# Optimization experiments

Hardware: AMD Instinct MI355X
Metric: run time of the kernel (lower is better)

## Reference

```python
import jax, jax.numpy as jnp
import numpy as np

L, B, D, H = 2048, 2, 1024, 16
HD = D // H
DFF = 4 * D
EPS = 1e-5


def layernorm(x, g, b):
    mu = jnp.mean(x, axis=-1, keepdims=True)
    var = jnp.mean((x - mu) ** 2, axis=-1, keepdims=True)
    return (x - mu) * jax.lax.rsqrt(var + EPS) * g + b


def setup_inputs() -> dict:
    key = jax.random.key(0)
    ks = jax.random.split(key, 12)
    s = 0.02
    return {
        "x": jax.random.normal(ks[0], (L, B, D), jnp.float32),
        "ln1_g": jnp.ones((D,), jnp.float32),
        "ln1_b": jnp.zeros((D,), jnp.float32),
        "w_attn": jax.random.normal(ks[1], (D, 3 * D), jnp.float32) * s,
        "b_attn": jnp.zeros((3 * D,), jnp.float32),
        "w_proj": jax.random.normal(ks[2], (D, D), jnp.float32) * s,
        "b_proj": jnp.zeros((D,), jnp.float32),
        "ln2_g": jnp.ones((D,), jnp.float32),
        "ln2_b": jnp.zeros((D,), jnp.float32),
        "w_fc": jax.random.normal(ks[3], (D, DFF), jnp.float32) * s,
        "b_fc": jnp.zeros((DFF,), jnp.float32),
        "w_out": jax.random.normal(ks[4], (DFF, D), jnp.float32) * s,
        "b_out": jnp.zeros((D,), jnp.float32),
    }


def reference(x, ln1_g, ln1_b, w_attn, b_attn, w_proj, b_proj,
              ln2_g, ln2_b, w_fc, b_fc, w_out, b_out):
    # x: [L, B, D]
    h = layernorm(x, ln1_g, ln1_b)
    qkv = h @ w_attn + b_attn                     # [L, B, 3D]
    qkv = jnp.transpose(qkv, (1, 0, 2))            # [B, L, 3D]
    q, k, v = jnp.split(qkv, 3, axis=-1)

    def split_heads(t):                            # [B, L, D] -> [B, H, L, hd]
        return jnp.transpose(t.reshape(B, L, H, HD), (0, 2, 1, 3))

    q, k, v = split_heads(q), split_heads(k), split_heads(v)
    # present: stack of (key, value), key in [B,H,L,hd] layout (post transpose-back)
    present = jnp.stack((k, v))                    # [2, B, H, L, hd]

    scores = jnp.einsum('bhqd,bhkd->bhqk', q, k) / jnp.sqrt(jnp.float32(HD))
    w = jax.nn.softmax(scores, axis=-1)
    a = jnp.einsum('bhqk,bhkd->bhqd', w, v)        # [B, H, L, hd]
    a = jnp.transpose(a, (0, 2, 1, 3)).reshape(B, L, D)
    a = a @ w_proj + b_proj                        # [B, L, D]
    a = jnp.transpose(a, (1, 0, 2))                # [L, B, D]

    x = x + a
    m = jax.nn.gelu(layernorm(x, ln2_g, ln2_b) @ w_fc + b_fc) @ w_out + b_out
    x = x + m
    return x, present
```

## Files before the change

kernel.cpp:

```cpp
#include <hip/hip_runtime.h>
#include <stdint.h>

#define L_SEQ 2048
#define BATCH 2
#define DIM   1024
#define NH    16
#define HDIM  64
#define DFF_  4096
#define ROWS  (L_SEQ*BATCH)

#define QSCALE 0.18033688011112042f

typedef __attribute__((ext_vector_type(8))) short  bf16x8;
typedef __attribute__((ext_vector_type(4))) float  floatx4;

__device__ __forceinline__ unsigned short f2bf(float f) {
    union { float f; uint32_t u; } x; x.f = f;
    uint32_t r = x.u + 0x7fffu + ((x.u >> 16) & 1u);
    return (unsigned short)(r >> 16);
}
__device__ __forceinline__ float bf2f(unsigned short b) {
    union { uint32_t u; float f; } x; x.u = ((uint32_t)b) << 16;
    return x.f;
}
__device__ __forceinline__ uint32_t fbits(float f) {
    union { float f; uint32_t u; } x; x.f = f; return x.u;
}

__device__ __forceinline__ void load_lds16(const unsigned short* g, unsigned short* l) {
    __builtin_amdgcn_global_load_lds(
        (const __attribute__((address_space(1))) unsigned int*)g,
        (__attribute__((address_space(3))) unsigned int*)l, 16, 0, 0);
}

__global__ __launch_bounds__(256)
void transpose_all(const float* __restrict__ s0, unsigned short* __restrict__ d0,
                   const float* __restrict__ s1, unsigned short* __restrict__ d1,
                   const float* __restrict__ s2, unsigned short* __restrict__ d2,
                   const float* __restrict__ s3, unsigned short* __restrict__ d3)
{
    const int id = blockIdx.x;
    const float* src; unsigned short* dst; int K, N, local;
    if (id < 3072)      { src = s0; dst = d0; K = 1024; N = 3072; local = id; }
    else if (id < 4096) { src = s1; dst = d1; K = 1024; N = 1024; local = id - 3072; }
    else if (id < 8192) { src = s2; dst = d2; K = 1024; N = 4096; local = id - 4096; }
    else                { src = s3; dst = d3; K = 4096; N = 1024; local = id - 8192; }
    const int nN = N >> 5;
    const int bk = (local / nN) * 32, bn = (local % nN) * 32;

    __shared__ float tile[32][36];
    const int t = threadIdx.x;
    const int r = t >> 3, c4 = (t & 7) * 4;
    *(float4*)&tile[r][c4] = *(const float4*)(src + (size_t)(bk + r) * N + bn + c4);
    __syncthreads();
    ushort4 o;
    o.x = f2bf(tile[c4 + 0][r]);
    o.y = f2bf(tile[c4 + 1][r]);
    o.z = f2bf(tile[c4 + 2][r]);
    o.w = f2bf(tile[c4 + 3][r]);
    *(ushort4*)(dst + (size_t)(bn + r) * K + bk + c4) = o;
}

template<int INBF16>
__global__ __launch_bounds__(256)
void ln_rows(const void* __restrict__ xin, const float* __restrict__ g,
             const float* __restrict__ bta, unsigned short* __restrict__ out)
{
    const int row = blockIdx.x;
    const int t = threadIdx.x;
    float4 v;
    if (INBF16) {
        const ushort4 u = ((const ushort4*)((const unsigned short*)xin + (size_t)row * DIM))[t];
        v.x = bf2f(u.x); v.y = bf2f(u.y); v.z = bf2f(u.z); v.w = bf2f(u.w);
    } else {
        v = ((const float4*)((const float*)xin + (size_t)row * DIM))[t];
    }
    float s  = v.x + v.y + v.z + v.w;
    float s2 = v.x*v.x + v.y*v.y + v.z*v.z + v.w*v.w;
#pragma unroll
    for (int d = 1; d < 64; d <<= 1) { s += __shfl_xor(s, d, 64); s2 += __shfl_xor(s2, d, 64); }
    __shared__ float ss[4], ss2[4];
    const int w = t >> 6, lane = t & 63;
    if (lane == 0) { ss[w] = s; ss2[w] = s2; }
    __syncthreads();
    s  = ss[0] + ss[1] + ss[2] + ss[3];
    s2 = ss2[0] + ss2[1] + ss2[2] + ss2[3];
    const float mu   = s * (1.0f / DIM);
    const float var  = s2 * (1.0f / DIM) - mu * mu;
    const float rstd = rsqrtf(var + 1e-5f);
    const float4 gv = ((const float4*)g)[t];
    const float4 bv = ((const float4*)bta)[t];
    ushort4 o;
    o.x = f2bf((v.x - mu) * rstd * gv.x + bv.x);
    o.y = f2bf((v.y - mu) * rstd * gv.y + bv.y);
    o.z = f2bf((v.z - mu) * rstd * gv.z + bv.z);
    o.w = f2bf((v.w - mu) * rstd * gv.w + bv.w);
    *(ushort4*)(out + (size_t)row * DIM + t * 4) = o;
}

template<int GELU, int RESID, int OUTBF16, int MI, int SPLITK>
__global__ __launch_bounds__(256)
void gemm_bt(const unsigned short* __restrict__ A,
             const unsigned short* __restrict__ Bt,
             const float* __restrict__ bias,
             const void* __restrict__ resid,
             void* __restrict__ outp,
             float* __restrict__ part,
             int M, int N, int K)
{
    __shared__ unsigned short As[MI * 32 * 32];
    __shared__ unsigned short Bs[128 * 32];
    const int t = threadIdx.x;
    const int w = t >> 6, lane = t & 63;
    const int quad = lane >> 4, l16 = lane & 15;
    const int wm = (w >> 1) * (MI * 16), wn = (w & 1) * 64;
    const int bm = blockIdx.x * (MI * 32), bn = blockIdx.y * 128;

    const int srow = lane >> 2;
    const int scol = (lane & 3) * 8;

    const unsigned short* Ab = A  + (size_t)bm * K;
    const unsigned short* Bb = Bt + (size_t)bn * K;

    floatx4 acc[MI][4] = {};

    const int kspan = (SPLITK > 1) ? (K / SPLITK) : K;
    const int k0    = (SPLITK > 1) ? blockIdx.z * kspan : 0;

    for (int kc = k0; kc < k0 + kspan; kc += 32) {
        __syncthreads();
#pragma unroll
        for (int i = 0; i < MI / 2; ++i) {
            const int r0 = (i * 4 + w) * 16;
            load_lds16(Ab + (size_t)(r0 + srow) * K + kc + scol, As + r0 * 32);
        }
#pragma unroll
        for (int i = 0; i < 2; ++i) {
            const int r0 = (i * 4 + w) * 16;
            load_lds16(Bb + (size_t)(r0 + srow) * K + kc + scol, Bs + r0 * 32);
        }
        __syncthreads();
        bf16x8 af[MI], bf[4];
#pragma unroll
        for (int i = 0; i < MI; ++i) af[i] = *(const bf16x8*)(As + (wm + i*16 + l16) * 32 + quad * 8);
#pragma unroll
        for (int j = 0; j < 4; ++j) bf[j] = *(const bf16x8*)(Bs + (wn + j*16 + l16) * 32 + quad * 8);
#pragma unroll
        for (int i = 0; i < MI; ++i)
#pragma unroll
            for (int j = 0; j < 4; ++j)
                acc[i][j] = __builtin_amdgcn_mfma_f32_16x16x32_bf16(af[i], bf[j], acc[i][j], 0, 0, 0);
    }

    if (SPLITK > 1 && blockIdx.z > 0) {
        float* po = part + (size_t)(blockIdx.z - 1) * ((size_t)M * N);
#pragma unroll
        for (int i = 0; i < MI; ++i)
#pragma unroll
            for (int j = 0; j < 4; ++j) {
                const int col = bn + wn + j*16 + l16;
#pragma unroll
                for (int r = 0; r < 4; ++r) {
                    const int row = bm + wm + i*16 + quad*4 + r;
                    po[(size_t)row * N + col] = acc[i][j][r];
                }
            }
        return;
    }

#pragma unroll
    for (int i = 0; i < MI; ++i) {
#pragma unroll
        for (int j = 0; j < 4; ++j) {
            const int col = bn + wn + j*16 + l16;
            const float bv = bias[col];
#pragma unroll
            for (int r = 0; r < 4; ++r) {
                const int row = bm + wm + i*16 + quad*4 + r;
                float v = acc[i][j][r] + bv;
                if (RESID == 1) v += ((const float*)resid)[(size_t)row * N + col];
                if (RESID == 2) v += bf2f(((const unsigned short*)resid)[(size_t)row * N + col]);
                if (GELU) {
                    const float u = v;
                    float c = 2.302204225929898f * (u + 0.044715f * u * u * u);
                    c = fminf(c, 80.f);
                    const float e = exp2f(c);
                    v = u * (e / (1.0f + e));
                }
                if (OUTBF16) ((unsigned short*)outp)[(size_t)row * N + col] = f2bf(v);
                else         ((float*)outp)[(size_t)row * N + col] = v;
            }
        }
    }
}

__global__ __launch_bounds__(256)
void splitk_add(const float* __restrict__ part, float* __restrict__ outp)
{
    const size_t i = ((size_t)blockIdx.x * 256 + threadIdx.x) * 4;
    float4 a = *(const float4*)(outp + i);
    const float4 p = *(const float4*)(part + i);
    a.x += p.x; a.y += p.y; a.z += p.z; a.w += p.w;
    *(float4*)(outp + i) = a;
}

__global__ __launch_bounds__(256)
void split_qkv(const unsigned short* __restrict__ qkv,
               unsigned short* __restrict__ q, unsigned short* __restrict__ k,
               float* __restrict__ present)
{
    const size_t idx = (size_t)blockIdx.x * 256 + threadIdx.x;
    const int g8  = idx & 7;
    const int l   = (idx >> 3) & 2047;
    const int bh  = (idx >> 14) & 31;
    const int sel = (int)(idx >> 19);
    const int b = bh >> 4, h = bh & 15;
    const unsigned short* src = qkv + (size_t)(l * BATCH + b) * (3 * DIM) + sel * DIM + h * HDIM + g8 * 8;
    const uint4 val = *(const uint4*)src;
    const unsigned short* sv = (const unsigned short*)&val;
    if (sel == 0) {
        unsigned short ov[8];
#pragma unroll
        for (int j = 0; j < 8; ++j) ov[j] = f2bf(bf2f(sv[j]) * QSCALE);
        *(uint4*)(q + ((size_t)bh * L_SEQ + l) * HDIM + g8 * 8) = *(uint4*)ov;
    } else {
        *(uint4*)(k + ((size_t)bh * L_SEQ + l) * HDIM + g8 * 8) = val;
        float* p = present + (((size_t)b * NH + h) * L_SEQ + l) * HDIM + (size_t)g8 * 8;
        float4 f0, f1;
        f0.x = bf2f(sv[0]); f0.y = bf2f(sv[1]); f0.z = bf2f(sv[2]); f0.w = bf2f(sv[3]);
        f1.x = bf2f(sv[4]); f1.y = bf2f(sv[5]); f1.z = bf2f(sv[6]); f1.w = bf2f(sv[7]);
        ((float4*)p)[0] = f0; ((float4*)p)[1] = f1;
    }
}

__global__ __launch_bounds__(256)
void transpose_v(const unsigned short* __restrict__ qkv, unsigned short* __restrict__ vt,
                 float* __restrict__ present)
{
    __shared__ unsigned short tile[64][72];
    const int lt = blockIdx.x;
    const int bh = blockIdx.y;
    const int b = bh >> 4, h = bh & 15;
    const int t = threadIdx.x;
#pragma unroll
    for (int i = 0; i < 2; ++i) {
        const int idx = i * 256 + t;
        const int l = idx >> 3, c = (idx & 7) * 8;
        const uint4 val =
            *(const uint4*)(qkv + (size_t)((lt * 64 + l) * BATCH + b) * (3 * DIM) + 2 * DIM + h * HDIM + c);
        *(uint4*)(&tile[l][c]) = val;
        const unsigned short* sv = (const unsigned short*)&val;
        float* p = present + ((((size_t)BATCH + b) * NH + h) * L_SEQ + lt * 64 + l) * HDIM + c;
        float4 f0, f1;
        f0.x = bf2f(sv[0]); f0.y = bf2f(sv[1]); f0.z = bf2f(sv[2]); f0.w = bf2f(sv[3]);
        f1.x = bf2f(sv[4]); f1.y = bf2f(sv[5]); f1.z = bf2f(sv[6]); f1.w = bf2f(sv[7]);
        ((float4*)p)[0] = f0; ((float4*)p)[1] = f1;
    }
    __syncthreads();
#pragma unroll
    for (int i = 0; i < 2; ++i) {
        const int idx = i * 256 + t;
        const int d = idx >> 3, l0 = (idx & 7) * 8;
        const int kk = l0 >> 3;
        ushort4 o[2];
        unsigned short* ov = (unsigned short*)o;
#pragma unroll
        for (int jj = 0; jj < 8; ++jj) {
            const int j = (jj + kk) & 7;
            ov[j] = tile[l0 + j][d];
        }
        *(uint4*)(vt + ((size_t)bh * HDIM + d) * L_SEQ + lt * 64 + l0) = *(uint4*)o;
    }
}

__global__ __launch_bounds__(256, 4)
void attn_kernel(const unsigned short* __restrict__ Q,
                 const unsigned short* __restrict__ Kk,
                 const unsigned short* __restrict__ Vt,
                 unsigned short* __restrict__ Opart,
                 float* __restrict__ Lpart)
{
    const int qt = blockIdx.x;
    const int ks = blockIdx.y;
    const int bh = blockIdx.z;
    const int b = bh >> 4, h = bh & 15;
    const int t = threadIdx.x, w = t >> 6, lane = t & 63;
    const int quad = lane >> 4, l16 = lane & 15;

    __shared__ unsigned short Ks[64][72];
    __shared__ unsigned short Vts[64][72];
    __shared__ unsigned short Ps[4][32][72];

    const size_t head_off = (size_t)bh * L_SEQ * HDIM;
    const int q_base = qt * 128 + w * 32;
    const int kt0 = ks * 1024;

    bf16x8 qf[2][2];
#pragma unroll
    for (int nf = 0; nf < 2; ++nf)
#pragma unroll
        for (int ds = 0; ds < 2; ++ds)
            qf[nf][ds] = *(const bf16x8*)(Q + head_off + (size_t)(q_base + nf*16 + l16) * HDIM + ds*32 + quad*8);

    const int sr = t >> 3;
    const int sc = (t & 7) * 8;

    floatx4 o[4][2] = {};
    float l_i[2] = {0.f, 0.f};

    for (int kt = kt0; kt < kt0 + 1024; kt += 64) {
        __syncthreads();
#pragma unroll
        for (int i = 0; i < 2; ++i) {
            const int row = sr + i * 32;
            *(uint4*)(&Ks[row][sc])  = *(const uint4*)(Kk + head_off + (size_t)(kt + row) * HDIM + sc);
            *(uint4*)(&Vts[row][sc]) = *(const uint4*)(Vt + head_off + (size_t)row * L_SEQ + kt + sc);
        }
        __syncthreads();

        floatx4 s[4][2] = {};
#pragma unroll
        for (int ds = 0; ds < 2; ++ds)
#pragma unroll
            for (int jt = 0; jt < 4; ++jt) {
                const bf16x8 kf = *(const bf16x8*)(&Ks[jt*16 + l16][ds*32 + quad*8]);
                s[jt][0] = __builtin_amdgcn_mfma_f32_16x16x32_bf16(kf, qf[0][ds], s[jt][0], 0, 0, 0);
                s[jt][1] = __builtin_amdgcn_mfma_f32_16x16x32_bf16(kf, qf[1][ds], s[jt][1], 0, 0, 0);
            }

#pragma unroll
        for (int nf = 0; nf < 2; ++nf)
#pragma unroll
            for (int jt = 0; jt < 4; ++jt) {
                const float p0 = exp2f(s[jt][nf][0]);
                const float p1 = exp2f(s[jt][nf][1]);
                const float p2 = exp2f(s[jt][nf][2]);
                const float p3 = exp2f(s[jt][nf][3]);
                l_i[nf] += (p0 + p1) + (p2 + p3);
                uint2 pk;
                pk.x = __builtin_amdgcn_perm(fbits(p1), fbits(p0), 0x07060302u);
                pk.y = __builtin_amdgcn_perm(fbits(p3), fbits(p2), 0x07060302u);
                *(uint2*)(&Ps[w][nf*16 + l16][jt*16 + quad*4]) = pk;
            }

#pragma unroll
        for (int kk = 0; kk < 2; ++kk) {
            const bf16x8 pf0 = *(const bf16x8*)(&Ps[w][l16]     [kk*32 + quad*8]);
            const bf16x8 pf1 = *(const bf16x8*)(&Ps[w][16 + l16][kk*32 + quad*8]);
#pragma unroll
            for (int dt = 0; dt < 4; ++dt) {
                const bf16x8 vf = *(const bf16x8*)(&Vts[dt*16 + l16][kk*32 + quad*8]);
                o[dt][0] = __builtin_amdgcn_mfma_f32_16x16x32_bf16(vf, pf0, o[dt][0], 0, 0, 0);
                o[dt][1] = __builtin_amdgcn_mfma_f32_16x16x32_bf16(vf, pf1, o[dt][1], 0, 0, 0);
            }
        }
    }

    unsigned short* Op = Opart + (size_t)ks * ROWS * DIM;
#pragma unroll
    for (int nf = 0; nf < 2; ++nf) {
        float l = l_i[nf];
        l += __shfl_xor(l, 16, 64);
        l += __shfl_xor(l, 32, 64);
        const int q = q_base + nf*16 + l16;
        if (quad == 0)
            Lpart[((size_t)ks * 32 + bh) * L_SEQ + q] = l;
#pragma unroll
        for (int dt = 0; dt < 4; ++dt) {
            ushort4 ov;
            ov.x = f2bf(o[dt][nf][0]); ov.y = f2bf(o[dt][nf][1]);
            ov.z = f2bf(o[dt][nf][2]); ov.w = f2bf(o[dt][nf][3]);
            *(ushort4*)(Op + (size_t)(q * BATCH + b) * DIM + h * HDIM + dt*16 + quad*4) = ov;
        }
    }
}

__global__ __launch_bounds__(256)
void attn_merge(const unsigned short* __restrict__ Opart,
                const float* __restrict__ Lpart,
                unsigned short* __restrict__ Aout)
{
    const int row = blockIdx.x;
    const int q = row >> 1, b = row & 1;
    const int t = threadIdx.x;
    const int col = t * 4;
    const int h = col >> 6;
    const int bh = b * 16 + h;
    const float l0 = Lpart[(size_t)bh * L_SEQ + q];
    const float l1 = Lpart[((size_t)32 + bh) * L_SEQ + q];
    const float inv = 1.0f / (l0 + l1);
    const ushort4 o0 = *(const ushort4*)(Opart + (size_t)row * DIM + col);
    const ushort4 o1 = *(const ushort4*)(Opart + (size_t)ROWS * DIM + (size_t)row * DIM + col);
    ushort4 ov;
    ov.x = f2bf((bf2f(o0.x) + bf2f(o1.x)) * inv);
    ov.y = f2bf((bf2f(o0.y) + bf2f(o1.y)) * inv);
    ov.z = f2bf((bf2f(o0.z) + bf2f(o1.z)) * inv);
    ov.w = f2bf((bf2f(o0.w) + bf2f(o1.w)) * inv);
    *(ushort4*)(Aout + (size_t)row * DIM + col) = ov;
}

extern "C" void kernel_launch(void* const* d_in, const int* in_sizes, int n_in,
                              void* d_out, int out_size, void* d_ws, size_t ws_size,
                              hipStream_t stream)
{
    const float* x      = (const float*)d_in[0];
    const float* ln1_g  = (const float*)d_in[1];
    const float* ln1_b  = (const float*)d_in[2];
    const float* w_attn = (const float*)d_in[3];
    const float* b_attn = (const float*)d_in[4];
    const float* w_proj = (const float*)d_in[5];
    const float* b_proj = (const float*)d_in[6];
    const float* ln2_g  = (const float*)d_in[7];
    const float* ln2_b  = (const float*)d_in[8];
    const float* w_fc   = (const float*)d_in[9];
    const float* b_fc   = (const float*)d_in[10];
    const float* w_out  = (const float*)d_in[11];
    const float* b_out  = (const float*)d_in[12];

    char* ws = (char*)d_ws;
    unsigned short* watT   = (unsigned short*)(ws + 0);
    unsigned short* wprojT = (unsigned short*)(ws + 6291456);
    unsigned short* wfcT   = (unsigned short*)(ws + 8388608);
    unsigned short* woutT  = (unsigned short*)(ws + 16777216);
    unsigned short* h      = (unsigned short*)(ws + 25165824);
    unsigned short* qkv    = (unsigned short*)(ws + 33554432);
    unsigned short* opart  = (unsigned short*)(ws + 33554432);
    float*          lpart  = (float*)(ws + 50331648);
    unsigned short* mws    = (unsigned short*)(ws + 33554432);
    unsigned short* qw     = (unsigned short*)(ws + 58720256);
    unsigned short* kw     = (unsigned short*)(ws + 67108864);
    unsigned short* vt     = (unsigned short*)(ws + 75497472);
    unsigned short* aw     = (unsigned short*)(ws + 83886080);
    unsigned short* x2     = (unsigned short*)(ws + 92274688);
    float*          kpart  = (float*)(ws + 75497472);

    float* xout    = (float*)d_out;
    float* present = (float*)d_out + 4194304;

    transpose_all<<<12288, 256, 0, stream>>>(w_attn, watT, w_proj, wprojT, w_fc, wfcT, w_out, woutT);

    ln_rows<0><<<ROWS, 256, 0, stream>>>(x, ln1_g, ln1_b, h);
    gemm_bt<0,0,1,4,1><<<dim3(32, 24), 256, 0, stream>>>(h, watT, b_attn, nullptr, qkv, nullptr, ROWS, 3*DIM, DIM);
    split_qkv<<<4096, 256, 0, stream>>>(qkv, qw, kw, present);
    transpose_v<<<dim3(32, 32), 256, 0, stream>>>(qkv, vt, present);
    attn_kernel<<<dim3(16, 2, 32), 256, 0, stream>>>(qw, kw, vt, opart, lpart);
    attn_merge<<<ROWS, 256, 0, stream>>>(opart, lpart, aw);
    gemm_bt<0,1,1,2,1><<<dim3(64, 8), 256, 0, stream>>>(aw, wprojT, b_proj, x, x2, nullptr, ROWS, DIM, DIM);
    ln_rows<1><<<ROWS, 256, 0, stream>>>(x2, ln2_g, ln2_b, h);
    gemm_bt<1,0,1,4,1><<<dim3(32, 32), 256, 0, stream>>>(h, wfcT, b_fc, nullptr, mws, nullptr, ROWS, DFF_, DIM);
    gemm_bt<0,2,0,4,2><<<dim3(32, 8, 2), 256, 0, stream>>>(mws, woutT, b_out, x2, xout, kpart, ROWS, DIM, DFF_);
    splitk_add<<<4096, 256, 0, stream>>>(kpart, xout);
}
```

Baseline: 418.6 us.

## Add 256x256-tile 8-wave pipelined GEMM for QKV and FC projections

Adds a new bf16 GEMM kernel with 256x256 output tiles, 512 threads, 128KB of double-buffered LDS with an XOR swizzle, and direct global-to-LDS loads. The K loop is split into four phases that interleave staging of the next tile with MFMA clusters, using priority raising and explicit waitcnt/barriers. Blocks are remapped so neighbouring workgroups are spread across XCDs. It replaces the QKV and FC GEMMs when the large dynamic LDS attribute can be set, aiming for higher data reuse and compute/load overlap, at the cost of one block per CU and only 192 or 256 blocks per launch.

Result: slower. 431.3 us (+3.0%).

```diff
diff --git a/kernel.cpp b/kernel.cpp
--- a/kernel.cpp
+++ b/kernel.cpp
@@ -194,6 +194,178 @@
     }
 }
 
+#define SWZ(p) ((p) ^ ((((p) >> 9) & 1) << 5))
+
+template<int GELU>
+__global__ __launch_bounds__(512)
+void gemm256(const unsigned short* __restrict__ A,
+             const unsigned short* __restrict__ Bt,
+             const float* __restrict__ bias,
+             unsigned short* __restrict__ outp,
+             int M, int N, int K, int nbx)
+{
+    extern __shared__ unsigned short lds[];
+    const int t = threadIdx.x;
+    const int w = t >> 6, lane = t & 63;
+    const int quad = lane >> 4, l16 = lane & 15;
+    const int wr = w >> 2, wc = w & 3;
+
+    const int nwg = gridDim.x;
+    const int cpx = nwg >> 3;
+    const int bid = (blockIdx.x & 7) * cpx + (blockIdx.x >> 3);
+    const int bm = (bid % nbx) * 256, bn = (bid / nbx) * 256;
+
+    const unsigned short* Ab = A  + (size_t)bm * K;
+    const unsigned short* Bb = Bt + (size_t)bn * K;
+
+    const int q0 = t * 16,        s0 = SWZ(q0);
+    const int q1 = (512 + t) * 16, s1 = SWZ(q1);
+    const int srow0 = s0 >> 7, scol0 = (s0 & 127) >> 1;
+    const int srow1 = s1 >> 7, scol1 = (s1 & 127) >> 1;
+
+#define STAGE(cb_, kt_, half_) do {                                                   \
+        const unsigned short* sb_ = ((half_) >= 2 ? Ab : Bb)                          \
+            + (size_t)(((half_) & 1) * 128) * K + (kt_) * 64;                         \
+        unsigned short* db_ = lds + (cb_) * 32768 + ((half_) >= 2 ? 0 : 16384)        \
+            + ((half_) & 1) * 8192 + w * 512;                                         \
+        load_lds16(sb_ + (size_t)srow0 * K + scol0, db_);                             \
+        load_lds16(sb_ + (size_t)srow1 * K + scol1, db_ + 4096);                      \
+    } while (0)
+
+#define PHASE_BAR  do { __builtin_amdgcn_s_barrier(); asm volatile("" ::: "memory"); } while (0)
+#define CL_PRE  do { asm volatile("s_waitcnt lgkmcnt(0)" ::: "memory"); \
+                     __builtin_amdgcn_sched_barrier(0); __builtin_amdgcn_s_setprio(1); } while (0)
+#define CL_POST do { __builtin_amdgcn_s_setprio(0); __builtin_amdgcn_sched_barrier(0); } while (0)
+
+    floatx4 acc[8][4] = {};
+    bf16x8 af[4][2], bf[4][2];
+    const int nt = K >> 6;
+
+    STAGE(0, 0, 0); STAGE(0, 0, 1); STAGE(0, 0, 2); STAGE(0, 0, 3);
+    STAGE(1, 1, 0);
+    asm volatile("s_waitcnt vmcnt(2)" ::: "memory");
+    PHASE_BAR;
+
+    for (int kt = 0; kt < nt; ++kt) {
+        const int cb = kt & 1;
+        const unsigned short* Al = lds + cb * 32768;
+        const unsigned short* Bl = lds + cb * 32768 + 16384;
+
+#pragma unroll
+        for (int mi = 0; mi < 4; ++mi)
+#pragma unroll
+            for (int ks = 0; ks < 2; ++ks) {
+                int p = (wr*128 + mi*16 + l16) * 128 + ks*64 + quad*16;
+                af[mi][ks] = *(const bf16x8*)((const char*)Al + SWZ(p));
+            }
+#pragma unroll
+        for (int nj = 0; nj < 4; ++nj)
+#pragma unroll
+            for (int ks = 0; ks < 2; ++ks) {
+                int p = (wc*64 + nj*16 + l16) * 128 + ks*64 + quad*16;
+                bf[nj][ks] = *(const bf16x8*)((const char*)Bl + SWZ(p));
+            }
+        if (kt + 1 < nt) STAGE((kt + 1) & 1, kt + 1, 1);
+        PHASE_BAR;
+        CL_PRE;
+#pragma unroll
+        for (int mi = 0; mi < 4; ++mi)
+#pragma unroll
+            for (int nj = 0; nj < 2; ++nj)
+#pragma unroll
+                for (int ks = 0; ks < 2; ++ks)
+                    acc[mi][nj] = __builtin_amdgcn_mfma_f32_16x16x32_bf16(af[mi][ks], bf[nj][ks], acc[mi][nj], 0, 0, 0);
+        CL_POST;
+        PHASE_BAR;
+
+        if (kt + 1 < nt) STAGE((kt + 1) & 1, kt + 1, 2);
+        PHASE_BAR;
+        CL_PRE;
+#pragma unroll
+        for (int mi = 0; mi < 4; ++mi)
+#pragma unroll
+            for (int nj = 2; nj < 4; ++nj)
+#pragma unroll
+                for (int ks = 0; ks < 2; ++ks)
+                    acc[mi][nj] = __builtin_amdgcn_mfma_f32_16x16x32_bf16(af[mi][ks], bf[nj][ks], acc[mi][nj], 0, 0, 0);
+        CL_POST;
+        PHASE_BAR;
+
+#pragma unroll
+        for (int mi = 0; mi < 4; ++mi)
+#pragma unroll
+            for (int ks = 0; ks < 2; ++ks) {
+                int p = (wr*128 + 64 + mi*16 + l16) * 128 + ks*64 + quad*16;
+                af[mi][ks] = *(const bf16x8*)((const char*)Al + SWZ(p));
+            }
+        if (kt + 1 < nt) STAGE((kt + 1) & 1, kt + 1, 3);
+        PHASE_BAR;
+        CL_PRE;
+#pragma unroll
+        for (int mi = 0; mi < 4; ++mi)
+#pragma unroll
+            for (int nj = 0; nj < 2; ++nj)
+#pragma unroll
+                for (int ks = 0; ks < 2; ++ks)
+                    acc[4 + mi][nj] = __builtin_amdgcn_mfma_f32_16x16x32_bf16(af[mi][ks], bf[nj][ks], acc[4 + mi][nj], 0, 0, 0);
+        CL_POST;
+        PHASE_BAR;
+
+        if (kt + 2 < nt) STAGE(cb, kt + 2, 0);
+        PHASE_BAR;
+        CL_PRE;
+#pragma unroll
+        for (int mi = 0; mi < 4; ++mi)
+#pragma unroll
+            for (int nj = 2; nj < 4; ++nj)
+#pragma unroll
+                for (int ks = 0; ks < 2; ++ks)
+                    acc[4 + mi][nj] = __builtin_amdgcn_mfma_f32_16x16x32_bf16(af[mi][ks], bf[nj][ks], acc[4 + mi][nj], 0, 0, 0);
+        CL_POST;
+        if (kt + 2 < nt)      { asm volatile("s_waitcnt vmcnt(2)" ::: "memory"); }
+        else if (kt + 1 < nt) { asm volatile("s_waitcnt vmcnt(0)" ::: "memory"); }
+        PHASE_BAR;
+    }
+
+#pragma unroll
+    for (int mi = 0; mi < 8; ++mi) {
+#pragma unroll
+        for (int nj = 0; nj < 4; ++nj) {
+            const int col = bn + wc*64 + nj*16 + l16;
+            const float bv = bias[col];
+#pragma unroll
+            for (int r = 0; r < 4; ++r) {
+                const int row = bm + wr*128 + mi*16 + quad*4 + r;
+                float v = acc[mi][nj][r] + bv;
+                if (GELU) {
+                    const float u = v;
+                    float c = 2.302204225929898f * (u + 0.044715f * u * u * u);
+                    c = fminf(c, 80.f);
+                    const float e = exp2f(c);
+                    v = u * (e / (1.0f + e));
+                }
+                outp[(size_t)row * N + col] = f2bf(v);
+            }
+        }
+    }
+#undef STAGE
+#undef PHASE_BAR
+#undef CL_PRE
+#undef CL_POST
+}
+
+static int g_big_lds_ok = 0;
+struct Gemm256Init {
+    Gemm256Init() {
+        hipError_t e1 = hipFuncSetAttribute(reinterpret_cast<const void*>(gemm256<0>),
+                                            hipFuncAttributeMaxDynamicSharedMemorySize, 131072);
+        hipError_t e2 = hipFuncSetAttribute(reinterpret_cast<const void*>(gemm256<1>),
+                                            hipFuncAttributeMaxDynamicSharedMemorySize, 131072);
+        g_big_lds_ok = (e1 == hipSuccess && e2 == hipSuccess) ? 1 : 0;
+    }
+};
+static Gemm256Init g_gemm256_init;
+
 __global__ __launch_bounds__(256)
 void splitk_add(const float* __restrict__ part, float* __restrict__ outp)
 {
@@ -440,14 +612,20 @@
     transpose_all<<<12288, 256, 0, stream>>>(w_attn, watT, w_proj, wprojT, w_fc, wfcT, w_out, woutT);
 
     ln_rows<0><<<ROWS, 256, 0, stream>>>(x, ln1_g, ln1_b, h);
-    gemm_bt<0,0,1,4,1><<<dim3(32, 24), 256, 0, stream>>>(h, watT, b_attn, nullptr, qkv, nullptr, ROWS, 3*DIM, DIM);
+    if (g_big_lds_ok)
+        gemm256<0><<<dim3(192), 512, 131072, stream>>>(h, watT, b_attn, qkv, ROWS, 3*DIM, DIM, 16);
+    else
+        gemm_bt<0,0,1,4,1><<<dim3(32, 24), 256, 0, stream>>>(h, watT, b_attn, nullptr, qkv, nullptr, ROWS, 3*DIM, DIM);
     split_qkv<<<4096, 256, 0, stream>>>(qkv, qw, kw, present);
     transpose_v<<<dim3(32, 32), 256, 0, stream>>>(qkv, vt, present);
     attn_kernel<<<dim3(16, 2, 32), 256, 0, stream>>>(qw, kw, vt, opart, lpart);
     attn_merge<<<ROWS, 256, 0, stream>>>(opart, lpart, aw);
     gemm_bt<0,1,1,2,1><<<dim3(64, 8), 256, 0, stream>>>(aw, wprojT, b_proj, x, x2, nullptr, ROWS, DIM, DIM);
     ln_rows<1><<<ROWS, 256, 0, stream>>>(x2, ln2_g, ln2_b, h);
-    gemm_bt<1,0,1,4,1><<<dim3(32, 32), 256, 0, stream>>>(h, wfcT, b_fc, nullptr, mws, nullptr, ROWS, DFF_, DIM);
+    if (g_big_lds_ok)
+        gemm256<1><<<dim3(256), 512, 131072, stream>>>(h, wfcT, b_fc, mws, ROWS, DFF_, DIM, 16);
+    else
+        gemm_bt<1,0,1,4,1><<<dim3(32, 32), 256, 0, stream>>>(h, wfcT, b_fc, nullptr, mws, nullptr, ROWS, DFF_, DIM);
     gemm_bt<0,2,0,4,2><<<dim3(32, 8, 2), 256, 0, stream>>>(mws, woutT, b_out, x2, xout, kpart, ROWS, DIM, DFF_);
     splitk_add<<<4096, 256, 0, stream>>>(kpart, xout);
 }
```

## Add 256x256-tile 512-thread GEMM for QKV and FC projections

Applied to the files above, without the earlier changes.

Adds a new bf16 MFMA GEMM kernel that uses 256x256 output tiles, 8 waves per block, swizzled LDS and double-buffered direct-to-LDS loads staggered between the A and B halves. It also remaps block IDs across 8 groups for cache locality, and it uses setprio and sched barriers around the MFMA clusters. The QKV and FC GEMMs now use this kernel in place of the older 128-tile one, aiming for more data reuse per block and better overlap of loads with compute. The larger tile gives fewer blocks (192 and 256), which may underfill the 256 CUs, and it raises register pressure.

New measurement: 412.8 us. Within noise of the previous version (-1.4%).

```diff
diff --git a/kernel.cpp b/kernel.cpp
--- a/kernel.cpp
+++ b/kernel.cpp
@@ -194,6 +194,152 @@
     }
 }
 
+#define SWZ32(p) ((p) ^ ((((p) >> 7) & 3) << 4))
+
+template<int GELU, int RESID, int OUTBF16, int SPLITK>
+__global__ __launch_bounds__(512, 2)
+void gemm256b(const unsigned short* __restrict__ A,
+              const unsigned short* __restrict__ Bt,
+              const float* __restrict__ bias,
+              const void* __restrict__ resid,
+              void* __restrict__ outp,
+              float* __restrict__ part,
+              int M, int N, int K, int nbx)
+{
+    __shared__ unsigned short lds[32768];
+    const int t = threadIdx.x;
+    const int w = t >> 6, lane = t & 63;
+    const int quad = lane >> 4, l16 = lane & 15;
+    const int wr = w >> 2, wc = w & 3;
+
+    const int nwg = gridDim.x;
+    const int cpx = nwg >> 3;
+    const int bid = (blockIdx.x & 7) * cpx + (blockIdx.x >> 3);
+    const int bm = (bid % nbx) * 256, bn = (bid / nbx) * 256;
+
+    const unsigned short* Ab = A  + (size_t)bm * K;
+    const unsigned short* Bb = Bt + (size_t)bn * K;
+
+    const int q0 = t * 16, q1 = 8192 + t * 16;
+    const int s0 = SWZ32(q0), s1 = SWZ32(q1);
+    const size_t aoff0 = (size_t)(s0 >> 6) * K + ((s0 & 63) >> 1);
+    const size_t aoff1 = (size_t)(s1 >> 6) * K + ((s1 & 63) >> 1);
+
+#define STG(dstE_, src_, kta_) do {                                        \
+        const unsigned short* g_ = (src_) + (size_t)(kta_) * 32;           \
+        load_lds16(g_ + aoff0, lds + (dstE_) + w * 512);                   \
+        load_lds16(g_ + aoff1, lds + (dstE_) + 4096 + w * 512);            \
+    } while (0)
+#define BARF    do { __builtin_amdgcn_s_barrier(); asm volatile("" ::: "memory"); } while (0)
+#define CL_PRE  do { asm volatile("s_waitcnt lgkmcnt(0)" ::: "memory");    \
+                     __builtin_amdgcn_sched_barrier(0);                    \
+                     __builtin_amdgcn_s_setprio(1); } while (0)
+#define CL_POST do { __builtin_amdgcn_s_setprio(0);                        \
+                     __builtin_amdgcn_sched_barrier(0); } while (0)
+
+    floatx4 acc[8][4] = {};
+    const int nt  = ((SPLITK > 1) ? (K / SPLITK) : K) >> 5;
+    const int ktb = (SPLITK > 1) ? blockIdx.y * nt : 0;
+
+    STG(0,            Ab, ktb);
+    STG(8192,         Bb, ktb);
+    STG(16384 + 8192, Bb, ktb + 1);
+    asm volatile("s_waitcnt vmcnt(2)" ::: "memory");
+    BARF;
+
+    for (int i = 0; i < nt; ++i) {
+        const int cb = i & 1;
+        const int i1 = (i + 1 < nt) ? i + 1 : nt - 1;
+        const int i2 = (i + 2 < nt) ? i + 2 : nt - 1;
+        const char* Abase = (const char*)lds + cb * 32768;
+        const char* Bbase = Abase + 16384;
+        bf16x8 af[4], bf[4];
+
+        STG((cb ^ 1) * 16384, Ab, ktb + i1);
+#pragma unroll
+        for (int mi = 0; mi < 4; ++mi) {
+            const int p = (wr * 128 + mi * 16 + l16) * 64 + quad * 16;
+            af[mi] = *(const bf16x8*)(Abase + SWZ32(p));
+        }
+#pragma unroll
+        for (int nj = 0; nj < 4; ++nj) {
+            const int p = (wc * 64 + nj * 16 + l16) * 64 + quad * 16;
+            bf[nj] = *(const bf16x8*)(Bbase + SWZ32(p));
+        }
+        BARF;
+        CL_PRE;
+#pragma unroll
+        for (int mi = 0; mi < 4; ++mi)
+#pragma unroll
+            for (int nj = 0; nj < 4; ++nj)
+                acc[mi][nj] = __builtin_amdgcn_mfma_f32_16x16x32_bf16(af[mi], bf[nj], acc[mi][nj], 0, 0, 0);
+        CL_POST;
+        BARF;
+
+        STG(cb * 16384 + 8192, Bb, ktb + i2);
+#pragma unroll
+        for (int mi = 0; mi < 4; ++mi) {
+            const int p = (wr * 128 + 64 + mi * 16 + l16) * 64 + quad * 16;
+            af[mi] = *(const bf16x8*)(Abase + SWZ32(p));
+        }
+        BARF;
+        CL_PRE;
+#pragma unroll
+        for (int mi = 0; mi < 4; ++mi)
+#pragma unroll
+            for (int nj = 0; nj < 4; ++nj)
+                acc[4 + mi][nj] = __builtin_amdgcn_mfma_f32_16x16x32_bf16(af[mi], bf[nj], acc[4 + mi][nj], 0, 0, 0);
+        CL_POST;
+        asm volatile("s_waitcnt vmcnt(2)" ::: "memory");
+        BARF;
+    }
+
+    if (SPLITK > 1 && blockIdx.y > 0) {
+        float* po = part + (size_t)(blockIdx.y - 1) * ((size_t)M * N);
+#pragma unroll
+        for (int mi = 0; mi < 8; ++mi)
+#pragma unroll
+            for (int nj = 0; nj < 4; ++nj) {
+                const int col = bn + wc * 64 + nj * 16 + l16;
+#pragma unroll
+                for (int r = 0; r < 4; ++r) {
+                    const int row = bm + wr * 128 + mi * 16 + quad * 4 + r;
+                    po[(size_t)row * N + col] = acc[mi][nj][r];
+                }
+            }
+        return;
+    }
+
+#pragma unroll
+    for (int mi = 0; mi < 8; ++mi) {
+#pragma unroll
+        for (int nj = 0; nj < 4; ++nj) {
+            const int col = bn + wc * 64 + nj * 16 + l16;
+            const float bv = bias[col];
+#pragma unroll
+            for (int r = 0; r < 4; ++r) {
+                const int row = bm + wr * 128 + mi * 16 + quad * 4 + r;
+                float v = acc[mi][nj][r] + bv;
+                if (RESID == 1) v += ((const float*)resid)[(size_t)row * N + col];
+                if (RESID == 2) v += bf2f(((const unsigned short*)resid)[(size_t)row * N + col]);
+                if (GELU) {
+                    const float u = v;
+                    float c = 2.302204225929898f * (u + 0.044715f * u * u * u);
+                    c = fminf(c, 80.f);
+                    const float e = exp2f(c);
+                    v = u * (e / (1.0f + e));
+                }
+                if (OUTBF16) ((unsigned short*)outp)[(size_t)row * N + col] = f2bf(v);
+                else         ((float*)outp)[(size_t)row * N + col] = v;
+            }
+        }
+    }
+#undef STG
+#undef BARF
+#undef CL_PRE
+#undef CL_POST
+}
+
 __global__ __launch_bounds__(256)
 void splitk_add(const float* __restrict__ part, float* __restrict__ outp)
 {
@@ -440,14 +586,14 @@
     transpose_all<<<12288, 256, 0, stream>>>(w_attn, watT, w_proj, wprojT, w_fc, wfcT, w_out, woutT);
 
     ln_rows<0><<<ROWS, 256, 0, stream>>>(x, ln1_g, ln1_b, h);
-    gemm_bt<0,0,1,4,1><<<dim3(32, 24), 256, 0, stream>>>(h, watT, b_attn, nullptr, qkv, nullptr, ROWS, 3*DIM, DIM);
+    gemm256b<0,0,1,1><<<dim3(192), 512, 0, stream>>>(h, watT, b_attn, nullptr, qkv, nullptr, ROWS, 3*DIM, DIM, 16);
     split_qkv<<<4096, 256, 0, stream>>>(qkv, qw, kw, present);
     transpose_v<<<dim3(32, 32), 256, 0, stream>>>(qkv, vt, present);
     attn_kernel<<<dim3(16, 2, 32), 256, 0, stream>>>(qw, kw, vt, opart, lpart);
     attn_merge<<<ROWS, 256, 0, stream>>>(opart, lpart, aw);
     gemm_bt<0,1,1,2,1><<<dim3(64, 8), 256, 0, stream>>>(aw, wprojT, b_proj, x, x2, nullptr, ROWS, DIM, DIM);
     ln_rows<1><<<ROWS, 256, 0, stream>>>(x2, ln2_g, ln2_b, h);
-    gemm_bt<1,0,1,4,1><<<dim3(32, 32), 256, 0, stream>>>(h, wfcT, b_fc, nullptr, mws, nullptr, ROWS, DFF_, DIM);
+    gemm256b<1,0,1,1><<<dim3(256), 512, 0, stream>>>(h, wfcT, b_fc, nullptr, mws, nullptr, ROWS, DFF_, DIM, 16);
     gemm_bt<0,2,0,4,2><<<dim3(32, 8, 2), 256, 0, stream>>>(mws, woutT, b_out, x2, xout, kpart, ROWS, DIM, DFF_);
     splitk_add<<<4096, 256, 0, stream>>>(kpart, xout);
 }
```

## Prefetch next K/V tile into registers and XOR-swizzle attention LDS tiles

Applied to the files above, without the earlier changes.

The attention kernel now issues global loads for the next K and V^T tile into registers before computing on the current tile, and writes them to LDS after the compute. This hides global load latency behind MFMA work. The padded LDS arrays are also replaced with unpadded 128-byte rows that use an XOR swizzle to avoid bank conflicts, which shrinks LDS use. In exchange the kernel holds more live registers, which may reduce occupancy under the launch bound of 4 blocks.

New measurement: 430.3 us. 1.03x slower.

```diff
diff --git a/kernel.cpp b/kernel.cpp
--- a/kernel.cpp
+++ b/kernel.cpp
@@ -273,6 +273,8 @@
     }
 }
 
+#define SWZA(p) ((p) ^ ((((p) >> 7) & 7) << 4))
+
 __global__ __launch_bounds__(256, 4)
 void attn_kernel(const unsigned short* __restrict__ Q,
                  const unsigned short* __restrict__ Kk,
@@ -287,9 +289,9 @@
     const int t = threadIdx.x, w = t >> 6, lane = t & 63;
     const int quad = lane >> 4, l16 = lane & 15;
 
-    __shared__ unsigned short Ks[64][72];
-    __shared__ unsigned short Vts[64][72];
-    __shared__ unsigned short Ps[4][32][72];
+    __shared__ unsigned short Ks[4096];
+    __shared__ unsigned short Vts[4096];
+    __shared__ unsigned short Ps[4][2048];
 
     const size_t head_off = (size_t)bh * L_SEQ * HDIM;
     const int q_base = qt * 128 + w * 32;
@@ -303,27 +305,43 @@
             qf[nf][ds] = *(const bf16x8*)(Q + head_off + (size_t)(q_base + nf*16 + l16) * HDIM + ds*32 + quad*8);
 
     const int sr = t >> 3;
-    const int sc = (t & 7) * 8;
+    const int c8 = t & 7;
+    const int sc = c8 * 8;
+    const int wb = sr * 128 + ((c8 * 16) ^ ((sr & 7) << 4));
+    const int wb2 = wb + 32 * 128;
+
+    uint4 kreg0, kreg1, vreg0, vreg1;
+
+#define LOAD_TILE(kt_) do {                                                              \
+        kreg0 = *(const uint4*)(Kk + head_off + (size_t)((kt_) + sr) * HDIM + sc);       \
+        kreg1 = *(const uint4*)(Kk + head_off + (size_t)((kt_) + sr + 32) * HDIM + sc);  \
+        vreg0 = *(const uint4*)(Vt + head_off + (size_t)sr * L_SEQ + (kt_) + sc);        \
+        vreg1 = *(const uint4*)(Vt + head_off + (size_t)(sr + 32) * L_SEQ + (kt_) + sc); \
+    } while (0)
+#define WRITE_TILE() do {                                                                \
+        *(uint4*)((char*)Ks + wb)   = kreg0;                                             \
+        *(uint4*)((char*)Ks + wb2)  = kreg1;                                             \
+        *(uint4*)((char*)Vts + wb)  = vreg0;                                             \
+        *(uint4*)((char*)Vts + wb2) = vreg1;                                             \
+    } while (0)
 
     floatx4 o[4][2] = {};
     float l_i[2] = {0.f, 0.f};
 
-    for (int kt = kt0; kt < kt0 + 1024; kt += 64) {
-        __syncthreads();
-#pragma unroll
-        for (int i = 0; i < 2; ++i) {
-            const int row = sr + i * 32;
-            *(uint4*)(&Ks[row][sc])  = *(const uint4*)(Kk + head_off + (size_t)(kt + row) * HDIM + sc);
-            *(uint4*)(&Vts[row][sc]) = *(const uint4*)(Vt + head_off + (size_t)row * L_SEQ + kt + sc);
-        }
-        __syncthreads();
+    LOAD_TILE(kt0);
+    WRITE_TILE();
+    __syncthreads();
+
+    for (int it = 0; it < 16; ++it) {
+        if (it + 1 < 16) LOAD_TILE(kt0 + (it + 1) * 64);
 
         floatx4 s[4][2] = {};
 #pragma unroll
         for (int ds = 0; ds < 2; ++ds)
 #pragma unroll
             for (int jt = 0; jt < 4; ++jt) {
-                const bf16x8 kf = *(const bf16x8*)(&Ks[jt*16 + l16][ds*32 + quad*8]);
+                const int p = (jt*16 + l16) * 128 + ds*64 + quad*16;
+                const bf16x8 kf = *(const bf16x8*)((const char*)Ks + SWZA(p));
                 s[jt][0] = __builtin_amdgcn_mfma_f32_16x16x32_bf16(kf, qf[0][ds], s[jt][0], 0, 0, 0);
                 s[jt][1] = __builtin_amdgcn_mfma_f32_16x16x32_bf16(kf, qf[1][ds], s[jt][1], 0, 0, 0);
             }
@@ -340,20 +358,28 @@
                 uint2 pk;
                 pk.x = __builtin_amdgcn_perm(fbits(p1), fbits(p0), 0x07060302u);
                 pk.y = __builtin_amdgcn_perm(fbits(p3), fbits(p2), 0x07060302u);
-                *(uint2*)(&Ps[w][nf*16 + l16][jt*16 + quad*4]) = pk;
+                const int q = nf*16 + l16;
+                const int kb = jt*32 + quad*8;
+                *(uint2*)((char*)Ps[w] + q*128 + (kb ^ ((q & 7) << 4))) = pk;
             }
 
 #pragma unroll
         for (int kk = 0; kk < 2; ++kk) {
-            const bf16x8 pf0 = *(const bf16x8*)(&Ps[w][l16]     [kk*32 + quad*8]);
-            const bf16x8 pf1 = *(const bf16x8*)(&Ps[w][16 + l16][kk*32 + quad*8]);
+            const int cbyte = kk*64 + quad*16;
+            const bf16x8 pf0 = *(const bf16x8*)((const char*)Ps[w] + l16*128      + (cbyte ^ ((l16 & 7) << 4)));
+            const bf16x8 pf1 = *(const bf16x8*)((const char*)Ps[w] + (16+l16)*128 + (cbyte ^ ((l16 & 7) << 4)));
 #pragma unroll
             for (int dt = 0; dt < 4; ++dt) {
-                const bf16x8 vf = *(const bf16x8*)(&Vts[dt*16 + l16][kk*32 + quad*8]);
+                const int p = (dt*16 + l16) * 128 + cbyte;
+                const bf16x8 vf = *(const bf16x8*)((const char*)Vts + SWZA(p));
                 o[dt][0] = __builtin_amdgcn_mfma_f32_16x16x32_bf16(vf, pf0, o[dt][0], 0, 0, 0);
                 o[dt][1] = __builtin_amdgcn_mfma_f32_16x16x32_bf16(vf, pf1, o[dt][1], 0, 0, 0);
             }
         }
+
+        __syncthreads();
+        if (it + 1 < 16) WRITE_TILE();
+        __syncthreads();
     }
 
     unsigned short* Op = Opart + (size_t)ks * ROWS * DIM;
@@ -373,6 +399,8 @@
             *(ushort4*)(Op + (size_t)(q * BATCH + b) * DIM + h * HDIM + dt*16 + quad*4) = ov;
         }
     }
+#undef LOAD_TILE
+#undef WRITE_TILE
 }
 
 __global__ __launch_bounds__(256)
```
